# Kernel optimization log

Measured on AMD Instinct MI355X. Metric: run time of the kernel, lower is better.

Reference implementation:

```python
import jax, jax.numpy as jnp
import numpy as np

DIM = 1024
NUM_HEADS = 16
HEAD_DIM = DIM // NUM_HEADS
B, S = 2, 2048


def setup_inputs() -> dict:
    key = jax.random.key(0)
    ks = jax.random.split(key, 12)
    sc = 1.0 / np.sqrt(DIM)
    inp = {
        'x': jax.random.normal(ks[0], (B, S, DIM), dtype=jnp.float32),
        'Wq': jax.random.normal(ks[1], (DIM, DIM), dtype=jnp.float32) * sc,
        'bq': jnp.zeros((DIM,), dtype=jnp.float32),
        'Wk': jax.random.normal(ks[2], (DIM, DIM), dtype=jnp.float32) * sc,
        'bk': jnp.zeros((DIM,), dtype=jnp.float32),
        'Wv': jax.random.normal(ks[3], (DIM, DIM), dtype=jnp.float32) * sc,
        'bv': jnp.zeros((DIM,), dtype=jnp.float32),
        'Wg1': jax.random.normal(ks[4], (DIM, DIM // 2), dtype=jnp.float32) * sc,
        'bg1': jnp.zeros((DIM // 2,), dtype=jnp.float32),
        'Wg2': jax.random.normal(ks[5], (DIM // 2, NUM_HEADS), dtype=jnp.float32) * (1.0 / np.sqrt(DIM // 2)),
        'bg2': jnp.zeros((NUM_HEADS,), dtype=jnp.float32),
        'Wo': jax.random.normal(ks[6], (DIM, DIM), dtype=jnp.float32) * sc,
        'bo': jnp.zeros((DIM,), dtype=jnp.float32),
    }
    return inp


def reference(x, Wq, bq, Wk, bk, Wv, bv, Wg1, bg1, Wg2, bg2, Wo, bo):
    b, s, dim = x.shape
    h, d = NUM_HEADS, HEAD_DIM
    # QKV projections -> (b, h, s, d)
    q = (x @ Wq + bq).reshape(b, s, h, d).transpose(0, 2, 1, 3)
    k = (x @ Wk + bk).reshape(b, s, h, d).transpose(0, 2, 1, 3)
    v = (x @ Wv + bv).reshape(b, s, h, d).transpose(0, 2, 1, 3)
    # raw attention scores (b, h, q, k)
    scores = jnp.einsum('bhqd,bhkd->bhqk', q, k) / np.sqrt(d)
    # superposition gate: per-(batch, token) softmax over heads -> (b, s, h)
    gate = jax.nn.softmax(jnp.tanh(x @ Wg1 + bg1) @ Wg2 + bg2, axis=-1)
    gate = gate.transpose(0, 2, 1)[..., None]  # (b, h, s, 1) -- per-query scale
    scores = scores * gate
    probs = jax.nn.softmax(scores, axis=-1)
    # dropout is identity at inference
    attended = jnp.einsum('bhqk,bhkd->bhqd', probs, v)
    attended = attended.transpose(0, 2, 1, 3).reshape(b, s, dim)
    return attended @ Wo + bo
```

## Files before the change

### kernel.cpp

```cpp
#include <hip/hip_runtime.h>
#include <math.h>

#define DIM    1024
#define NHEADS 16
#define HDIM   64
#define BATCH  2
#define SEQ    2048
#define TOK    (BATCH * SEQ)

typedef unsigned short ushort;
typedef __attribute__((ext_vector_type(8))) short  short8;
typedef __attribute__((ext_vector_type(4))) float  f32x4;
typedef __attribute__((ext_vector_type(4))) unsigned short us4;

__device__ __forceinline__ ushort f2bf(float f) {
    unsigned u = __float_as_uint(f);
    u += 0x7fffu + ((u >> 16) & 1u);
    return (ushort)(u >> 16);
}
__device__ __forceinline__ float bf2f(ushort h) {
    return __uint_as_float(((unsigned)h) << 16);
}

__device__ __forceinline__ void gload16(const void* g, void* lds) {
    __builtin_amdgcn_global_load_lds(
        (const __attribute__((address_space(1))) unsigned int*)g,
        (__attribute__((address_space(3))) unsigned int*)lds, 16, 0, 0);
}

__global__ __launch_bounds__(256) void split_hl(
    const float* __restrict__ in, ushort* __restrict__ hi, ushort* __restrict__ lo)
{
    const int i = blockIdx.x * 256 + threadIdx.x;
    float4 v = ((const float4*)in)[i];
    us4 h, l;
    h.x = f2bf(v.x); l.x = f2bf(v.x - bf2f(h.x));
    h.y = f2bf(v.y); l.y = f2bf(v.y - bf2f(h.y));
    h.z = f2bf(v.z); l.z = f2bf(v.z - bf2f(h.z));
    h.w = f2bf(v.w); l.w = f2bf(v.w - bf2f(h.w));
    ((us4*)hi)[i] = h;
    ((us4*)lo)[i] = l;
}

__device__ __forceinline__ void tsplit_body(
    const float* __restrict__ in, ushort* __restrict__ hiT, ushort* __restrict__ loT,
    int K, int N, int k0, int n0)
{
    __shared__ float t[32][33];
    const int x = threadIdx.x & 31, y = threadIdx.x >> 5;
#pragma unroll
    for (int r = 0; r < 4; ++r)
        t[y + r * 8][x] = in[(size_t)(k0 + y + r * 8) * N + n0 + x];
    __syncthreads();
#pragma unroll
    for (int r = 0; r < 4; ++r) {
        const int row = y + r * 8;
        const float v = t[x][row];
        const ushort h = f2bf(v);
        const size_t o = (size_t)(n0 + row) * K + k0 + x;
        hiT[o] = h;
        loT[o] = f2bf(v - bf2f(h));
    }
}

__global__ __launch_bounds__(256) void wsplitT(
    const float* __restrict__ W0, const float* __restrict__ W1,
    const float* __restrict__ W2, const float* __restrict__ W3,
    const float* __restrict__ Wg1,
    ushort* __restrict__ hiT, ushort* __restrict__ loT,
    ushort* __restrict__ g1hiT, ushort* __restrict__ g1loT)
{
    const int z = blockIdx.z;
    if (z < 4) {
        const float* in = (z == 0) ? W0 : (z == 1) ? W1 : (z == 2) ? W2 : W3;
        tsplit_body(in, hiT + (size_t)z * DIM * DIM, loT + (size_t)z * DIM * DIM,
                    DIM, DIM, blockIdx.y * 32, blockIdx.x * 32);
    } else {
        if (blockIdx.x >= 16) return;
        tsplit_body(Wg1, g1hiT, g1loT, DIM, 512, blockIdx.y * 32, blockIdx.x * 32);
    }
}

template<int MREP>
__device__ __forceinline__ void mgemm_core(
    const ushort* __restrict__ Ahi, const ushort* __restrict__ Alo,
    const ushort* __restrict__ BThi, const ushort* __restrict__ BTlo,
    const float* __restrict__ bias, int act, int store, int npass,
    float* __restrict__ Cf, ushort* __restrict__ Ch, ushort* __restrict__ Cl,
    int ldc, int row0, int col0, ushort* ldsA, ushort* ldsB)
{
    const int tid  = threadIdx.x;
    const int lane = tid & 63;
    const int wid  = tid >> 6;
    const int wr   = wid >> 1;
    const int wc   = wid & 1;
    const int l15  = lane & 15;
    const int l4   = lane >> 4;

    f32x4 acc[MREP][4];
#pragma unroll
    for (int m = 0; m < MREP; ++m)
#pragma unroll
        for (int n = 0; n < 4; ++n) acc[m][n] = (f32x4){0.f, 0.f, 0.f, 0.f};

    const int trow = wid * 8 + (lane >> 3);
    const int swz  = ((lane & 7) ^ (lane >> 3)) * 8;

    for (int ph = 0; ph < npass; ++ph) {
        const ushort* Ap = (ph == 1) ? Alo : Ahi;
        const ushort* Bp = (ph == 2) ? BTlo : BThi;
        const ushort* Asrc = Ap + (size_t)(row0 + trow) * 1024 + swz;
        const ushort* Bsrc = Bp + (size_t)(col0 + trow) * 1024 + swz;

        for (int k0 = 0; k0 < 1024; k0 += 64) {
            __syncthreads();
#pragma unroll
            for (int r = 0; r < MREP; ++r)
                gload16(Asrc + (size_t)r * 32 * 1024 + k0, &ldsA[(wid * 8 + r * 32) * 64]);
#pragma unroll
            for (int r = 0; r < 4; ++r)
                gload16(Bsrc + (size_t)r * 32 * 1024 + k0, &ldsB[(wid * 8 + r * 32) * 64]);
            __syncthreads();

#pragma unroll
            for (int s = 0; s < 2; ++s) {
                short8 a[MREP], b[4];
#pragma unroll
                for (int m = 0; m < MREP; ++m) {
                    const int row = wr * (MREP * 16) + m * 16 + l15;
                    a[m] = *(const short8*)&ldsA[row * 64 + (((s * 4 + l4) ^ (row & 7)) * 8)];
                }
#pragma unroll
                for (int n = 0; n < 4; ++n) {
                    const int row = wc * 64 + n * 16 + l15;
                    b[n] = *(const short8*)&ldsB[row * 64 + (((s * 4 + l4) ^ (row & 7)) * 8)];
                }
#pragma unroll
                for (int m = 0; m < MREP; ++m)
#pragma unroll
                    for (int n = 0; n < 4; ++n)
                        acc[m][n] = __builtin_amdgcn_mfma_f32_16x16x32_bf16(
                            a[m], b[n], acc[m][n], 0, 0, 0);
            }
        }
    }

#pragma unroll
    for (int m = 0; m < MREP; ++m)
#pragma unroll
        for (int n = 0; n < 4; ++n) {
            const int c = col0 + wc * 64 + n * 16 + l15;
            const float bc = bias[c];
            f32x4 v = acc[m][n];
            if (store == 4) {
                const int r0 = row0 + wr * (MREP * 16) + m * 16 + l4 * 4;
                const int bb = r0 >> 11, s0 = r0 & (SEQ - 1);
                const int hh = c >> 6,  d = c & (HDIM - 1);
                us4 pk;
#pragma unroll
                for (int rg = 0; rg < 4; ++rg) pk[rg] = f2bf(v[rg] + bc);
                *(us4*)&Ch[(((size_t)bb * NHEADS + hh) * HDIM + d) * SEQ + s0] = pk;
                continue;
            }
#pragma unroll
            for (int rg = 0; rg < 4; ++rg) {
                const int r = row0 + wr * (MREP * 16) + m * 16 + l4 * 4 + rg;
                float o = v[rg] + bc;
                if (act == 1) o = tanhf(o);
                if (store == 0) {
                    Cf[(size_t)r * ldc + c] = o;
                } else if (store == 1) {
                    const int bb = r >> 11, s = r & (SEQ - 1);
                    const int hh = c >> 6,  d = c & (HDIM - 1);
                    Cf[(((size_t)bb * NHEADS + hh) * SEQ + s) * HDIM + d] = o;
                } else {
                    const int bb = r >> 11, s = r & (SEQ - 1);
                    const int hh = c >> 6,  d = c & (HDIM - 1);
                    const size_t off = (((size_t)bb * NHEADS + hh) * SEQ + s) * HDIM + d;
                    const ushort hb = f2bf(o);
                    Ch[off] = hb;
                    if (store == 2) Cl[off] = f2bf(o - bf2f(hb));
                }
            }
        }
}

__global__ __launch_bounds__(256) void mgemm_fused(
    const ushort* __restrict__ xhi, const ushort* __restrict__ xlo,
    const ushort* __restrict__ WThi, const ushort* __restrict__ WTlo,
    const ushort* __restrict__ Wg1Thi, const ushort* __restrict__ Wg1Tlo,
    const float* __restrict__ bq, const float* __restrict__ bk,
    const float* __restrict__ bv, const float* __restrict__ bg1,
    float* __restrict__ qb, ushort* __restrict__ khB, ushort* __restrict__ klB,
    ushort* __restrict__ vTB, float* __restrict__ Hb)
{
    __shared__ ushort ldsA[128 * 64];
    __shared__ ushort ldsB[128 * 64];

    const int y = blockIdx.y;
    const ushort *Bh, *Bl;
    const float* bias;
    int act = 0, store, npass, ldc = DIM, col0;
    float* Cf = nullptr;
    ushort *Ch = nullptr, *Cl = nullptr;

    if (y < 24) {
        const int sel = y >> 3;
        col0 = (y & 7) * 128;
        const size_t off = (size_t)sel * DIM * DIM;
        Bh = WThi + off; Bl = WTlo + off;
        if (sel == 0)      { bias = bq; store = 1; npass = 3; Cf = qb; }
        else if (sel == 1) { bias = bk; store = 2; npass = 3; Ch = khB; Cl = klB; }
        else               { bias = bv; store = 4; npass = 1; Ch = vTB; }
    } else {
        col0 = (y - 24) * 128;
        Bh = Wg1Thi; Bl = Wg1Tlo; bias = bg1;
        act = 1; store = 0; npass = 2; Cf = Hb; ldc = 512;
    }
    mgemm_core<4>(xhi, xlo, Bh, Bl, bias, act, store, npass, Cf, Ch, Cl, ldc,
                  blockIdx.x * 128, col0, ldsA, ldsB);
}

__global__ __launch_bounds__(256) void mgemm_out(
    const ushort* __restrict__ Ahi, const ushort* __restrict__ Alo,
    const ushort* __restrict__ BThi, const ushort* __restrict__ BTlo,
    const float* __restrict__ bias, float* __restrict__ Cf)
{
    __shared__ ushort ldsA[64 * 64];
    __shared__ ushort ldsB[128 * 64];
    mgemm_core<2>(Ahi, Alo, BThi, BTlo, bias, 0, 0, 2, Cf, nullptr, nullptr, DIM,
                  blockIdx.x * 64, blockIdx.y * 128, ldsA, ldsB);
}

__global__ __launch_bounds__(256) void gate2_kernel(
    const float* __restrict__ H, const float* __restrict__ Wg2,
    const float* __restrict__ bg2, float* __restrict__ gate)
{
    const int wave = threadIdx.x >> 6;
    const int lane = threadIdx.x & 63;
    const int t    = blockIdx.x * 4 + wave;
    const int hh   = lane >> 2;
    const int p    = lane & 3;

    const float* Hrow = H + (size_t)t * 512;
    float s = 0.f;
    const int k0 = p * 128;
#pragma unroll 8
    for (int kk = 0; kk < 128; kk++)
        s = __builtin_fmaf(Hrow[k0 + kk], Wg2[(k0 + kk) * NHEADS + hh], s);
    s += __shfl_xor(s, 1);
    s += __shfl_xor(s, 2);
    s += bg2[hh];

    float mx = s;
    mx = fmaxf(mx, __shfl_xor(mx, 4));
    mx = fmaxf(mx, __shfl_xor(mx, 8));
    mx = fmaxf(mx, __shfl_xor(mx, 16));
    mx = fmaxf(mx, __shfl_xor(mx, 32));
    const float e = __expf(s - mx);
    float den = e;
    den += __shfl_xor(den, 4);
    den += __shfl_xor(den, 8);
    den += __shfl_xor(den, 16);
    den += __shfl_xor(den, 32);
    if (p == 0) gate[(size_t)t * NHEADS + hh] = e / den;
}

__global__ __launch_bounds__(256, 2) void flash_mfma(
    const float* __restrict__ q,
    const ushort* __restrict__ khi, const ushort* __restrict__ klo,
    const ushort* __restrict__ vT,
    const float* __restrict__ gate,
    ushort* __restrict__ att_hi, ushort* __restrict__ att_lo)
{
    __shared__ ushort lds[20480];
    ushort* Khi = lds;
    ushort* Klo = lds + 4096;
    ushort* Vt  = lds + 8192;

    const int tid  = threadIdx.x;
    const int lane = tid & 63;
    const int wid  = tid >> 6;
    const int l15  = lane & 15;
    const int l4   = lane >> 4;
    const int qt   = blockIdx.x;
    const int bh   = blockIdx.y;
    const int b    = bh >> 4, h = bh & 15;

    ushort* Pwv = lds + 12288 + wid * 2048;

    short8 qhf[2][2], qlf[2][2];
#pragma unroll
    for (int n = 0; n < 2; n++) {
        const int qrow = qt * 128 + wid * 32 + n * 16 + l15;
        const float g = gate[(size_t)(b * SEQ + qrow) * NHEADS + h] * 0.125f;
        const float* qr = q + ((size_t)bh * SEQ + qrow) * HDIM;
#pragma unroll
        for (int kc = 0; kc < 2; kc++) {
            const int d0 = kc * 32 + l4 * 8;
            float4 f0 = *(const float4*)(qr + d0);
            float4 f1 = *(const float4*)(qr + d0 + 4);
            float vals[8] = {f0.x, f0.y, f0.z, f0.w, f1.x, f1.y, f1.z, f1.w};
            short8 hh, ll;
#pragma unroll
            for (int j = 0; j < 8; j++) {
                const float gq = vals[j] * g;
                const ushort hb = f2bf(gq);
                hh[j] = (short)hb;
                ll[j] = (short)f2bf(gq - bf2f(hb));
            }
            qhf[n][kc] = hh;
            qlf[n][kc] = ll;
        }
    }

    const ushort* Ksrc_h = khi + (size_t)bh * SEQ * HDIM;
    const ushort* Ksrc_l = klo + (size_t)bh * SEQ * HDIM;
    const ushort* Vsrc   = vT  + (size_t)bh * HDIM * SEQ;

    float m_[2] = {-INFINITY, -INFINITY};
    float l_[2] = {0.f, 0.f};
    f32x4 O[2][4];
#pragma unroll
    for (int mq = 0; mq < 2; mq++)
#pragma unroll
        for (int nd = 0; nd < 4; nd++) O[mq][nd] = (f32x4){0.f, 0.f, 0.f, 0.f};

    for (int kt = 0; kt < SEQ / 64; kt++) {
        __syncthreads();
#pragma unroll
        for (int p = 0; p < 2; p++) {
            const int r   = wid * 16 + p * 8 + (lane >> 3);
            const int cs  = ((lane & 7) ^ (r & 7)) * 8;
            const int dst = (wid * 16 + p * 8) * 64 + lane * 8;
            gload16(Ksrc_h + (size_t)(kt * 64 + r) * HDIM + cs, &Khi[dst]);
            gload16(Ksrc_l + (size_t)(kt * 64 + r) * HDIM + cs, &Klo[dst]);
            gload16(Vsrc + (size_t)r * SEQ + kt * 64 + cs, &Vt[dst]);
        }
        __syncthreads();

        f32x4 ST[4][2];
#pragma unroll
        for (int mt = 0; mt < 4; mt++)
#pragma unroll
            for (int n = 0; n < 2; n++) ST[mt][n] = (f32x4){0.f, 0.f, 0.f, 0.f};

#pragma unroll
        for (int kc = 0; kc < 2; kc++) {
            short8 ka[4];
#pragma unroll
            for (int mt = 0; mt < 4; mt++) {
                const int row = mt * 16 + l15;
                ka[mt] = *(const short8*)&Khi[row * 64 + (((kc * 4 + l4) ^ (row & 7)) * 8)];
            }
#pragma unroll
            for (int mt = 0; mt < 4; mt++)
#pragma unroll
                for (int n = 0; n < 2; n++)
                    ST[mt][n] = __builtin_amdgcn_mfma_f32_16x16x32_bf16(
                        ka[mt], qhf[n][kc], ST[mt][n], 0, 0, 0);
#pragma unroll
            for (int mt = 0; mt < 4; mt++)
#pragma unroll
                for (int n = 0; n < 2; n++)
                    ST[mt][n] = __builtin_amdgcn_mfma_f32_16x16x32_bf16(
                        ka[mt], qlf[n][kc], ST[mt][n], 0, 0, 0);
        }
#pragma unroll
        for (int kc = 0; kc < 2; kc++) {
            short8 ka[4];
#pragma unroll
            for (int mt = 0; mt < 4; mt++) {
                const int row = mt * 16 + l15;
                ka[mt] = *(const short8*)&Klo[row * 64 + (((kc * 4 + l4) ^ (row & 7)) * 8)];
            }
#pragma unroll
            for (int mt = 0; mt < 4; mt++)
#pragma unroll
                for (int n = 0; n < 2; n++)
                    ST[mt][n] = __builtin_amdgcn_mfma_f32_16x16x32_bf16(
                        ka[mt], qhf[n][kc], ST[mt][n], 0, 0, 0);
        }

        float scn[2];
#pragma unroll
        for (int n = 0; n < 2; n++) {
            float rm = fmaxf(fmaxf(ST[0][n][0], ST[0][n][1]), fmaxf(ST[0][n][2], ST[0][n][3]));
#pragma unroll
            for (int mt = 1; mt < 4; mt++) {
                rm = fmaxf(rm, fmaxf(fmaxf(ST[mt][n][0], ST[mt][n][1]),
                                     fmaxf(ST[mt][n][2], ST[mt][n][3])));
            }
            rm = fmaxf(rm, __shfl_xor(rm, 16));
            rm = fmaxf(rm, __shfl_xor(rm, 32));
            const float mn = fmaxf(m_[n], rm);
            scn[n] = __expf(m_[n] - mn);
            m_[n] = mn;
            float ps = 0.f;
#pragma unroll
            for (int mt = 0; mt < 4; mt++)
#pragma unroll
                for (int rg = 0; rg < 4; rg++) {
                    const float e = __expf(ST[mt][n][rg] - mn);
                    ST[mt][n][rg] = e;
                    ps += e;
                }
            ps += __shfl_xor(ps, 16);
            ps += __shfl_xor(ps, 32);
            l_[n] = l_[n] * scn[n] + ps;

            const int qq = n * 16 + l15;
#pragma unroll
            for (int mt = 0; mt < 4; mt++) {
                const unsigned lo32 = (unsigned)f2bf(ST[mt][n][0]) |
                                      ((unsigned)f2bf(ST[mt][n][1]) << 16);
                const unsigned hi32 = (unsigned)f2bf(ST[mt][n][2]) |
                                      ((unsigned)f2bf(ST[mt][n][3]) << 16);
                const unsigned long long pk = (unsigned long long)lo32 |
                                              ((unsigned long long)hi32 << 32);
                const int slot = (mt * 2 + (l4 >> 1)) ^ (qq & 7);
                *(unsigned long long*)&Pwv[qq * 64 + slot * 8 + (l4 & 1) * 4] = pk;
            }
        }

#pragma unroll
        for (int mq = 0; mq < 2; mq++)
#pragma unroll
            for (int rg = 0; rg < 4; rg++) {
                const float s = __shfl(scn[mq], l4 * 4 + rg);
#pragma unroll
                for (int nd = 0; nd < 4; nd++) O[mq][nd][rg] *= s;
            }

        asm volatile("s_waitcnt lgkmcnt(0)" ::: "memory");
        __builtin_amdgcn_sched_barrier(0);

#pragma unroll
        for (int kc2 = 0; kc2 < 2; kc2++) {
            short8 ap[2];
#pragma unroll
            for (int mq = 0; mq < 2; mq++) {
                const int qq = mq * 16 + l15;
                ap[mq] = *(const short8*)&Pwv[qq * 64 + (((kc2 * 4 + l4) ^ (qq & 7)) * 8)];
            }
#pragma unroll
            for (int nd = 0; nd < 4; nd++) {
                const int dd = nd * 16 + l15;
                const short8 bv = *(const short8*)&Vt[dd * 64 + (((kc2 * 4 + l4) ^ (dd & 7)) * 8)];
#pragma unroll
                for (int mq = 0; mq < 2; mq++)
                    O[mq][nd] = __builtin_amdgcn_mfma_f32_16x16x32_bf16(
                        ap[mq], bv, O[mq][nd], 0, 0, 0);
            }
        }
    }

#pragma unroll
    for (int mq = 0; mq < 2; mq++)
#pragma unroll
        for (int rg = 0; rg < 4; rg++) {
            const float linv = 1.f / __shfl(l_[mq], l4 * 4 + rg);
            const int s = qt * 128 + wid * 32 + mq * 16 + l4 * 4 + rg;
#pragma unroll
            for (int nd = 0; nd < 4; nd++) {
                const float o = O[mq][nd][rg] * linv;
                const ushort hb = f2bf(o);
                const size_t off = (size_t)(b * SEQ + s) * DIM + h * HDIM + nd * 16 + l15;
                att_hi[off] = hb;
                att_lo[off] = f2bf(o - bf2f(hb));
            }
        }
}

extern "C" void kernel_launch(void* const* d_in, const int* in_sizes, int n_in,
                              void* d_out, int out_size, void* d_ws, size_t ws_size,
                              hipStream_t stream)
{
    const float* x   = (const float*)d_in[0];
    const float* Wq  = (const float*)d_in[1];
    const float* bq  = (const float*)d_in[2];
    const float* Wk  = (const float*)d_in[3];
    const float* bk  = (const float*)d_in[4];
    const float* Wv  = (const float*)d_in[5];
    const float* bv  = (const float*)d_in[6];
    const float* Wg1 = (const float*)d_in[7];
    const float* bg1 = (const float*)d_in[8];
    const float* Wg2 = (const float*)d_in[9];
    const float* bg2 = (const float*)d_in[10];
    const float* Wo  = (const float*)d_in[11];
    const float* bo  = (const float*)d_in[12];
    float* out = (float*)d_out;

    char* p = (char*)d_ws;
    float*  qb    = (float*)p;   p += (size_t)TOK * DIM * 4;
    ushort* khB   = (ushort*)p;  p += (size_t)TOK * DIM * 2;
    ushort* klB   = (ushort*)p;  p += (size_t)TOK * DIM * 2;
    ushort* vTB   = (ushort*)p;  p += (size_t)TOK * DIM * 2;
    float*  Hb    = (float*)p;   p += (size_t)TOK * 512 * 4;
    float*  gateb = (float*)p;   p += (size_t)TOK * NHEADS * 4;
    ushort* xhi   = (ushort*)p;  p += (size_t)TOK * DIM * 2;
    ushort* xlo   = (ushort*)p;  p += (size_t)TOK * DIM * 2;
    ushort* atth  = (ushort*)p;  p += (size_t)TOK * DIM * 2;
    ushort* attl  = (ushort*)p;  p += (size_t)TOK * DIM * 2;
    ushort* WThi  = (ushort*)p;  p += (size_t)4 * DIM * DIM * 2;
    ushort* WTlo  = (ushort*)p;  p += (size_t)4 * DIM * DIM * 2;
    ushort* Wg1Thi= (ushort*)p;  p += (size_t)512 * DIM * 2;
    ushort* Wg1Tlo= (ushort*)p;  p += (size_t)512 * DIM * 2;

    split_hl<<<TOK * DIM / 4 / 256, 256, 0, stream>>>(x, xhi, xlo);

    wsplitT<<<dim3(32, 32, 5), 256, 0, stream>>>(
        Wq, Wk, Wv, Wo, Wg1, WThi, WTlo, Wg1Thi, Wg1Tlo);

    mgemm_fused<<<dim3(32, 28), 256, 0, stream>>>(
        xhi, xlo, WThi, WTlo, Wg1Thi, Wg1Tlo,
        bq, bk, bv, bg1, qb, khB, klB, vTB, Hb);

    gate2_kernel<<<dim3(TOK / 4), 256, 0, stream>>>(Hb, Wg2, bg2, gateb);

    flash_mfma<<<dim3(SEQ / 128, BATCH * NHEADS), 256, 0, stream>>>(
        qb, khB, klB, vTB, gateb, atth, attl);

    mgemm_out<<<dim3(64, 8), 256, 0, stream>>>(
        atth, attl, WThi + (size_t)3 * DIM * DIM, WTlo + (size_t)3 * DIM * DIM,
        bo, out);
}
```

Baseline: 349.0 us.

## Double-buffer K/V tiles in flash attention, lazy rescale, bf16 Q storage

The flash attention kernel now double-buffers its K-hi, K-lo and V tiles in LDS. It issues the global-to-LDS loads for the next tile before computing on the current one and waits with vmcnt instead of two full syncthreads per tile. Online-softmax rescaling of the output accumulator is skipped unless some row's max grows by more than a threshold of 8. The projection GEMM stores Q as a bf16 hi/lo pair instead of fp32, and score packing uses the hardware v_cvt_pk_bf16_f32 instruction. In exchange, LDS use grows from 40 KB to 64 KB per block, which may reduce occupancy, and the lazy rescale changes numerics slightly.

```diff
diff --git a/kernel.cpp b/kernel.cpp
--- a/kernel.cpp
+++ b/kernel.cpp
@@ -20,6 +20,11 @@
 }
 __device__ __forceinline__ float bf2f(ushort h) {
     return __uint_as_float(((unsigned)h) << 16);
+}
+__device__ __forceinline__ unsigned cvt_pk_bf16(float a, float b) {
+    unsigned r;
+    asm("v_cvt_pk_bf16_f32 %0, %1, %2" : "=v"(r) : "v"(a), "v"(b));
+    return r;
 }
 
 __device__ __forceinline__ void gload16(const void* g, void* lds) {
@@ -191,7 +196,8 @@
     const ushort* __restrict__ Wg1Thi, const ushort* __restrict__ Wg1Tlo,
     const float* __restrict__ bq, const float* __restrict__ bk,
     const float* __restrict__ bv, const float* __restrict__ bg1,
-    float* __restrict__ qb, ushort* __restrict__ khB, ushort* __restrict__ klB,
+    ushort* __restrict__ qhB, ushort* __restrict__ qlB,
+    ushort* __restrict__ khB, ushort* __restrict__ klB,
     ushort* __restrict__ vTB, float* __restrict__ Hb)
 {
     __shared__ ushort ldsA[128 * 64];
@@ -209,7 +215,7 @@
         col0 = (y & 7) * 128;
         const size_t off = (size_t)sel * DIM * DIM;
         Bh = WThi + off; Bl = WTlo + off;
-        if (sel == 0)      { bias = bq; store = 1; npass = 3; Cf = qb; }
+        if (sel == 0)      { bias = bq; store = 2; npass = 3; Ch = qhB; Cl = qlB; }
         else if (sel == 1) { bias = bk; store = 2; npass = 3; Ch = khB; Cl = klB; }
         else               { bias = bv; store = 4; npass = 1; Ch = vTB; }
     } else {
@@ -267,16 +273,13 @@
 }
 
 __global__ __launch_bounds__(256, 2) void flash_mfma(
-    const float* __restrict__ q,
+    const ushort* __restrict__ qhi, const ushort* __restrict__ qlo,
     const ushort* __restrict__ khi, const ushort* __restrict__ klo,
     const ushort* __restrict__ vT,
     const float* __restrict__ gate,
     ushort* __restrict__ att_hi, ushort* __restrict__ att_lo)
 {
-    __shared__ ushort lds[20480];
-    ushort* Khi = lds;
-    ushort* Klo = lds + 4096;
-    ushort* Vt  = lds + 8192;
+    __shared__ ushort lds[32768];
 
     const int tid  = threadIdx.x;
     const int lane = tid & 63;
@@ -287,27 +290,26 @@
     const int bh   = blockIdx.y;
     const int b    = bh >> 4, h = bh & 15;
 
-    ushort* Pwv = lds + 12288 + wid * 2048;
+    ushort* Pwv = lds + 24576 + wid * 2048;
 
     short8 qhf[2][2], qlf[2][2];
 #pragma unroll
     for (int n = 0; n < 2; n++) {
         const int qrow = qt * 128 + wid * 32 + n * 16 + l15;
         const float g = gate[(size_t)(b * SEQ + qrow) * NHEADS + h] * 0.125f;
-        const float* qr = q + ((size_t)bh * SEQ + qrow) * HDIM;
+        const size_t qoff = ((size_t)bh * SEQ + qrow) * HDIM;
 #pragma unroll
         for (int kc = 0; kc < 2; kc++) {
             const int d0 = kc * 32 + l4 * 8;
-            float4 f0 = *(const float4*)(qr + d0);
-            float4 f1 = *(const float4*)(qr + d0 + 4);
-            float vals[8] = {f0.x, f0.y, f0.z, f0.w, f1.x, f1.y, f1.z, f1.w};
+            short8 h8 = *(const short8*)&qhi[qoff + d0];
+            short8 l8 = *(const short8*)&qlo[qoff + d0];
             short8 hh, ll;
 #pragma unroll
             for (int j = 0; j < 8; j++) {
-                const float gq = vals[j] * g;
-                const ushort hb = f2bf(gq);
+                const float t = (bf2f((ushort)h8[j]) + bf2f((ushort)l8[j])) * g;
+                const ushort hb = f2bf(t);
                 hh[j] = (short)hb;
-                ll[j] = (short)f2bf(gq - bf2f(hb));
+                ll[j] = (short)f2bf(t - bf2f(hb));
             }
             qhf[n][kc] = hh;
             qlf[n][kc] = ll;
@@ -326,18 +328,31 @@
 #pragma unroll
         for (int nd = 0; nd < 4; nd++) O[mq][nd] = (f32x4){0.f, 0.f, 0.f, 0.f};
 
-    for (int kt = 0; kt < SEQ / 64; kt++) {
-        __syncthreads();
+    auto STAGE = [&](int bufOff, int kt) {
 #pragma unroll
         for (int p = 0; p < 2; p++) {
             const int r   = wid * 16 + p * 8 + (lane >> 3);
             const int cs  = ((lane & 7) ^ (r & 7)) * 8;
-            const int dst = (wid * 16 + p * 8) * 64 + lane * 8;
-            gload16(Ksrc_h + (size_t)(kt * 64 + r) * HDIM + cs, &Khi[dst]);
-            gload16(Ksrc_l + (size_t)(kt * 64 + r) * HDIM + cs, &Klo[dst]);
-            gload16(Vsrc + (size_t)r * SEQ + kt * 64 + cs, &Vt[dst]);
-        }
-        __syncthreads();
+            ushort* dst = lds + bufOff + (wid * 16 + p * 8) * 64 + lane * 8;
+            gload16(Ksrc_h + (size_t)(kt * 64 + r) * HDIM + cs, dst);
+            gload16(Ksrc_l + (size_t)(kt * 64 + r) * HDIM + cs, dst + 4096);
+            gload16(Vsrc + (size_t)r * SEQ + kt * 64 + cs, dst + 8192);
+        }
+    };
+
+    auto TILE = [&](int kt, int curOff, bool notLast) {
+        if (notLast) {
+            STAGE(curOff ^ 12288, kt + 1);
+            asm volatile("s_waitcnt vmcnt(6)" ::: "memory");
+        } else {
+            asm volatile("s_waitcnt vmcnt(0)" ::: "memory");
+        }
+        __builtin_amdgcn_s_barrier();
+        __builtin_amdgcn_sched_barrier(0);
+
+        const ushort* Khi = lds + curOff;
+        const ushort* Klo = Khi + 4096;
+        const ushort* Vt  = Khi + 8192;
 
         f32x4 ST[4][2];
 #pragma unroll
@@ -383,19 +398,28 @@
         }
 
         float scn[2];
+        bool resc[2];
 #pragma unroll
         for (int n = 0; n < 2; n++) {
             float rm = fmaxf(fmaxf(ST[0][n][0], ST[0][n][1]), fmaxf(ST[0][n][2], ST[0][n][3]));
 #pragma unroll
-            for (int mt = 1; mt < 4; mt++) {
+            for (int mt = 1; mt < 4; mt++)
                 rm = fmaxf(rm, fmaxf(fmaxf(ST[mt][n][0], ST[mt][n][1]),
                                      fmaxf(ST[mt][n][2], ST[mt][n][3])));
-            }
             rm = fmaxf(rm, __shfl_xor(rm, 16));
             rm = fmaxf(rm, __shfl_xor(rm, 32));
-            const float mn = fmaxf(m_[n], rm);
-            scn[n] = __expf(m_[n] - mn);
-            m_[n] = mn;
+
+            resc[n] = !__all(rm <= m_[n] + 8.0f);
+            float mn;
+            if (resc[n]) {
+                mn = fmaxf(m_[n], rm);
+                scn[n] = __expf(m_[n] - mn);
+                m_[n] = mn;
+            } else {
+                mn = m_[n];
+                scn[n] = 1.0f;
+            }
+
             float ps = 0.f;
 #pragma unroll
             for (int mt = 0; mt < 4; mt++)
@@ -412,10 +436,8 @@
             const int qq = n * 16 + l15;
 #pragma unroll
             for (int mt = 0; mt < 4; mt++) {
-                const unsigned lo32 = (unsigned)f2bf(ST[mt][n][0]) |
-                                      ((unsigned)f2bf(ST[mt][n][1]) << 16);
-                const unsigned hi32 = (unsigned)f2bf(ST[mt][n][2]) |
-                                      ((unsigned)f2bf(ST[mt][n][3]) << 16);
+                const unsigned lo32 = cvt_pk_bf16(ST[mt][n][0], ST[mt][n][1]);
+                const unsigned hi32 = cvt_pk_bf16(ST[mt][n][2], ST[mt][n][3]);
                 const unsigned long long pk = (unsigned long long)lo32 |
                                               ((unsigned long long)hi32 << 32);
                 const int slot = (mt * 2 + (l4 >> 1)) ^ (qq & 7);
@@ -423,14 +445,16 @@
             }
         }
 
-#pragma unroll
-        for (int mq = 0; mq < 2; mq++)
-#pragma unroll
-            for (int rg = 0; rg < 4; rg++) {
-                const float s = __shfl(scn[mq], l4 * 4 + rg);
-#pragma unroll
-                for (int nd = 0; nd < 4; nd++) O[mq][nd][rg] *= s;
-            }
+        if (resc[0] | resc[1]) {
+#pragma unroll
+            for (int mq = 0; mq < 2; mq++)
+#pragma unroll
+                for (int rg = 0; rg < 4; rg++) {
+                    const float s = __shfl(scn[mq], l4 * 4 + rg);
+#pragma unroll
+                    for (int nd = 0; nd < 4; nd++) O[mq][nd][rg] *= s;
+                }
+        }
 
         asm volatile("s_waitcnt lgkmcnt(0)" ::: "memory");
         __builtin_amdgcn_sched_barrier(0);
@@ -453,6 +477,13 @@
                         ap[mq], bv, O[mq][nd], 0, 0, 0);
             }
         }
+        __builtin_amdgcn_s_barrier();
+    };
+
+    STAGE(0, 0);
+    for (int kt2 = 0; kt2 < SEQ / 64; kt2 += 2) {
+        TILE(kt2,     0,     true);
+        TILE(kt2 + 1, 12288, kt2 + 1 < SEQ / 64 - 1);
     }
 
 #pragma unroll
@@ -492,7 +523,8 @@
     float* out = (float*)d_out;
 
     char* p = (char*)d_ws;
-    float*  qb    = (float*)p;   p += (size_t)TOK * DIM * 4;
+    ushort* qhB   = (ushort*)p;  p += (size_t)TOK * DIM * 2;
+    ushort* qlB   = (ushort*)p;  p += (size_t)TOK * DIM * 2;
     ushort* khB   = (ushort*)p;  p += (size_t)TOK * DIM * 2;
     ushort* klB   = (ushort*)p;  p += (size_t)TOK * DIM * 2;
     ushort* vTB   = (ushort*)p;  p += (size_t)TOK * DIM * 2;
@@ -514,12 +546,12 @@
 
     mgemm_fused<<<dim3(32, 28), 256, 0, stream>>>(
         xhi, xlo, WThi, WTlo, Wg1Thi, Wg1Tlo,
-        bq, bk, bv, bg1, qb, khB, klB, vTB, Hb);
+        bq, bk, bv, bg1, qhB, qlB, khB, klB, vTB, Hb);
 
     gate2_kernel<<<dim3(TOK / 4), 256, 0, stream>>>(Hb, Wg2, bg2, gateb);
 
     flash_mfma<<<dim3(SEQ / 128, BATCH * NHEADS), 256, 0, stream>>>(
-        qb, khB, klB, vTB, gateb, atth, attl);
+        qhB, qlB, khB, klB, vTB, gateb, atth, attl);
 
     mgemm_out<<<dim3(64, 8), 256, 0, stream>>>(
         atth, attl, WThi + (size_t)3 * DIM * DIM, WTlo + (size_t)3 * DIM * DIM,
```

Result: faster. 331.6 us (-5.0%).
